# Kernel tuning notes

Measured on AMD Instinct MI355X. Metric: run time of the kernel, lower is better.

Reference implementation:

```python
import jax, jax.numpy as jnp
import numpy as np
from jax import lax

B, T_IN, T_OUT = 32, 256, 500
N_MEL, ENC_DIM = 80, 512
ATT_RNN, DEC_RNN, PRENET, ATT_DIM = 1024, 1024, 256, 128
LOC_F, LOC_K = 32, 31
P_ATT_DROP, P_DEC_DROP = 0.1, 0.1


def setup_inputs() -> dict:
    key = jax.random.key(0)
    ks = jax.random.split(key, 24)
    rn = lambda k, s, sc=0.02: jax.random.normal(k, s, dtype=jnp.float32) * sc
    inp = {}
    inp['memory'] = jax.random.normal(ks[0], (B, T_IN, ENC_DIM), dtype=jnp.float32)
    inp['decoder_inputs'] = jax.random.normal(ks[1], (B, N_MEL, T_OUT), dtype=jnp.float32)
    inp['memory_lengths'] = jax.random.randint(ks[2], (B,), T_IN // 2, T_IN + 1)
    inp['prenet_w1'] = rn(ks[3], (PRENET, N_MEL))
    inp['prenet_w2'] = rn(ks[4], (PRENET, PRENET))
    inp['att_w_ih'] = rn(ks[5], (4 * ATT_RNN, PRENET + ENC_DIM))
    inp['att_w_hh'] = rn(ks[6], (4 * ATT_RNN, ATT_RNN))
    inp['att_b_ih'] = jnp.zeros((4 * ATT_RNN,), jnp.float32)
    inp['att_b_hh'] = jnp.zeros((4 * ATT_RNN,), jnp.float32)
    inp['query_w'] = rn(ks[7], (ATT_DIM, ATT_RNN))
    inp['memory_w'] = rn(ks[8], (ATT_DIM, ENC_DIM))
    inp['v_w'] = rn(ks[9], (1, ATT_DIM))
    inp['loc_conv_w'] = rn(ks[10], (LOC_F, 2, LOC_K))
    inp['loc_dense_w'] = rn(ks[11], (ATT_DIM, LOC_F))
    inp['dec_w_ih'] = rn(ks[12], (4 * DEC_RNN, ATT_RNN + ENC_DIM))
    inp['dec_w_hh'] = rn(ks[13], (4 * DEC_RNN, DEC_RNN))
    inp['dec_b_ih'] = jnp.zeros((4 * DEC_RNN,), jnp.float32)
    inp['dec_b_hh'] = jnp.zeros((4 * DEC_RNN,), jnp.float32)
    inp['proj_w'] = rn(ks[14], (N_MEL, DEC_RNN + ENC_DIM))
    inp['proj_b'] = jnp.zeros((N_MEL,), jnp.float32)
    inp['gate_w'] = rn(ks[15], (1, DEC_RNN + ENC_DIM))
    inp['gate_b'] = jnp.zeros((1,), jnp.float32)
    return inp


def _lstm_cell(x, h, c, w_ih, w_hh, b_ih, b_hh):
    gates = x @ w_ih.T + b_ih + h @ w_hh.T + b_hh
    i, f, g, o = jnp.split(gates, 4, axis=-1)
    c2 = jax.nn.sigmoid(f) * c + jax.nn.sigmoid(i) * jnp.tanh(g)
    h2 = jax.nn.sigmoid(o) * jnp.tanh(c2)
    return h2, c2


def _dropout_masks():
    # deterministic dropout masks (training=True semantics), keep-prob scaled
    kd = jax.random.key(1)
    k1, k2, k3, k4 = jax.random.split(kd, 4)
    m1 = jax.random.bernoulli(k1, 0.5, (T_OUT + 1, B, PRENET)).astype(jnp.float32) / 0.5
    m2 = jax.random.bernoulli(k2, 0.5, (T_OUT + 1, B, PRENET)).astype(jnp.float32) / 0.5
    ma = jax.random.bernoulli(k3, 1 - P_ATT_DROP, (T_OUT, B, ATT_RNN)).astype(jnp.float32) / (1 - P_ATT_DROP)
    md = jax.random.bernoulli(k4, 1 - P_DEC_DROP, (T_OUT, B, DEC_RNN)).astype(jnp.float32) / (1 - P_DEC_DROP)
    return m1, m2, ma, md


def _decode(memory, decoder_inputs, memory_lengths, prenet_w1, prenet_w2,
            att_w_ih, att_w_hh, att_b_ih, att_b_hh, query_w, memory_w, v_w,
            loc_conv_w, loc_dense_w, dec_w_ih, dec_w_hh, dec_b_ih, dec_b_hh,
            proj_w, proj_b, gate_w, gate_b):
    pm1, pm2, att_drop, dec_drop = _dropout_masks()
    processed_memory = jnp.einsum('bte,ae->bta', memory, memory_w)  # (B,T_in,128)
    pad_mask = jnp.arange(T_IN)[None, :] >= memory_lengths[:, None]  # True = padded

    # teacher-forced decoder inputs: (B,n_mel,T) -> (T,B,n_mel), prepend go frame
    dec_in = jnp.transpose(decoder_inputs, (2, 0, 1))
    dec_in = jnp.concatenate([jnp.zeros((1, B, N_MEL), dec_in.dtype), dec_in], 0)
    # prenet (relu + dropout p=0.5, always training)
    x = jax.nn.relu(dec_in @ prenet_w1.T) * pm1
    x = jax.nn.relu(x @ prenet_w2.T) * pm2
    prenet_out = x[:T_OUT]  # (T,B,256)

    pad = (LOC_K - 1) // 2

    def attention(att_h, aw, aw_cum):
        pq = att_h @ query_w.T  # (B,128)
        awc = jnp.stack([aw, aw_cum], axis=1)  # (B,2,T_in)
        loc = lax.conv_general_dilated(awc, loc_conv_w, (1,), [(pad, pad)],
                                       dimension_numbers=('NCH', 'OIH', 'NCH'))  # (B,32,T_in)
        loc = jnp.einsum('bft,af->bta', loc, loc_dense_w)  # (B,T_in,128)
        energies = jnp.tanh(pq[:, None, :] + loc + processed_memory) @ v_w[0]  # (B,T_in)
        energies = jnp.where(pad_mask, -jnp.inf, energies)
        w = jax.nn.softmax(energies, axis=1)
        ctx = jnp.einsum('bt,bte->be', w, memory)  # (B,512)
        return ctx, w

    def step(carry, xs):
        ah, ac, dh, dc, aw, aw_cum, ctx = carry
        pn, adm, ddm = xs
        cell_in = jnp.concatenate([pn, ctx], axis=-1)  # (B,768)
        ah, ac = _lstm_cell(cell_in, ah, ac, att_w_ih, att_w_hh, att_b_ih, att_b_hh)
        ah = ah * adm
        ctx, aw = attention(ah, aw, aw_cum)
        aw_cum = aw_cum + aw
        din = jnp.concatenate([ah, ctx], axis=-1)  # (B,1536)
        dh, dc = _lstm_cell(din, dh, dc, dec_w_ih, dec_w_hh, dec_b_ih, dec_b_hh)
        dh = dh * ddm
        dhac = jnp.concatenate([dh, ctx], axis=-1)  # (B,1536)
        mel = dhac @ proj_w.T + proj_b  # (B,80)
        gate = (dhac @ gate_w.T + gate_b)[:, 0]  # (B,)
        return (ah, ac, dh, dc, aw, aw_cum, ctx), (mel, gate, aw)

    z = lambda d: jnp.zeros((B, d), jnp.float32)
    init = (z(ATT_RNN), z(ATT_RNN), z(DEC_RNN), z(DEC_RNN),
            jnp.zeros((B, T_IN), jnp.float32), jnp.zeros((B, T_IN), jnp.float32), z(ENC_DIM))
    _, (mels, gates, aligns) = lax.scan(step, init, (prenet_out, att_drop, dec_drop))

    mel_outputs = jnp.transpose(mels, (1, 2, 0))   # (B, n_mel, T_out)
    gate_outputs = gates.T                          # (B, T_out)
    alignments = jnp.transpose(aligns, (1, 0, 2))   # (B, T_out, T_in)
    return mel_outputs, gate_outputs, alignments


def reference(memory, decoder_inputs, memory_lengths, prenet_w1, prenet_w2,
              att_w_ih, att_w_hh, att_b_ih, att_b_hh, query_w, memory_w, v_w,
              loc_conv_w, loc_dense_w, dec_w_ih, dec_w_hh, dec_b_ih, dec_b_hh,
              proj_w, proj_b, gate_w, gate_b):
    return _decode(memory, decoder_inputs, memory_lengths, prenet_w1, prenet_w2,
                   att_w_ih, att_w_hh, att_b_ih, att_b_hh, query_w, memory_w, v_w,
                   loc_conv_w, loc_dense_w, dec_w_ih, dec_w_hh, dec_b_ih, dec_b_hh,
                   proj_w, proj_b, gate_w, gate_b)
```

## Files before the change

kernel.cpp:

```cpp
#include <hip/hip_runtime.h>
#include <math.h>
#include <string.h>

#define TOUT 500
#define AOFF 1296000
#define GOFF 1280000
#define TF_BITS_XOR 1

typedef float f32x4 __attribute__((ext_vector_type(4)));
typedef short bf16x8 __attribute__((ext_vector_type(8)));
typedef unsigned short ushort4_t __attribute__((ext_vector_type(4)));
typedef unsigned u32x4 __attribute__((ext_vector_type(4)));

struct Params {
  const float *memory, *dec_in, *pw1, *pw2, *awih, *awhh, *abih, *abhh;
  const float *qw, *mw, *vw, *lcw, *ldw, *dwih, *dwhh, *dbih, *dbhh;
  const float *pjw, *pjb, *gw, *gb;
  const int* mlen;
  float* out;
  unsigned short *ahb0, *ahb1, *dhb0, *dhb1, *ctxb0, *ctxb1;
  unsigned *slots;
  unsigned *flags;
  float *x1, *w1t, *w2t, *mwt, *ldwt, *ba, *bd;
  unsigned short *pre_bf, *pm_bf, *mem_t, *qw_bf, *wpa, *wpd;
  unsigned *mma, *mmd, *mm1, *mm2;
};

__host__ __device__ inline void tf_block(unsigned k0, unsigned k1, unsigned x0, unsigned x1,
                                         unsigned& o0, unsigned& o1) {
  unsigned ks2 = k0 ^ k1 ^ 0x1BD11BDAu;
  x0 += k0; x1 += k1;
#define TFR(r) { x0 += x1; x1 = (x1 << r) | (x1 >> (32 - r)); x1 ^= x0; }
  TFR(13) TFR(15) TFR(26) TFR(6)
  x0 += k1;  x1 += ks2 + 1u;
  TFR(17) TFR(29) TFR(16) TFR(24)
  x0 += ks2; x1 += k0 + 2u;
  TFR(13) TFR(15) TFR(26) TFR(6)
  x0 += k0;  x1 += k1 + 3u;
  TFR(17) TFR(29) TFR(16) TFR(24)
  x0 += k1;  x1 += ks2 + 4u;
  TFR(13) TFR(15) TFR(26) TFR(6)
  x0 += ks2; x1 += k0 + 5u;
#undef TFR
  o0 = x0; o1 = x1;
}

__device__ inline float sigf(float x) { return 1.f / (1.f + __expf(-x)); }
__device__ inline float tanh_fast(float x) {
  float ax = fabsf(x);
  float t = __expf(-2.f * ax);
  float r = (1.f - t) / (1.f + t);
  return copysignf(r, x);
}
__device__ inline unsigned short f2bf(float f) {
  unsigned u = __float_as_uint(f);
  unsigned r = (u + 0x7FFFu + ((u >> 16) & 1u)) >> 16;
  return (unsigned short)r;
}
__device__ inline float bf2f(unsigned short u) {
  return __uint_as_float((unsigned)u << 16);
}

__device__ inline unsigned long long ld_coh64(const void* ptr) {
  return __hip_atomic_load((unsigned long long*)ptr, __ATOMIC_RELAXED, __HIP_MEMORY_SCOPE_SYSTEM);
}
__device__ inline unsigned ld_coh32(const unsigned* ptr) {
  return __hip_atomic_load(ptr, __ATOMIC_RELAXED, __HIP_MEMORY_SCOPE_SYSTEM);
}
__device__ inline void st_coh32(unsigned* ptr, unsigned v) {
  __hip_atomic_store(ptr, v, __ATOMIC_RELAXED, __HIP_MEMORY_SCOPE_SYSTEM);
}

template<bool COH>
__device__ __forceinline__ u32x4 ld16(const void* ptr) {
  u32x4 r;
// ... 143 lines not shown
  int b = wg >> 4, tc = wg & 15;
  int tid = threadIdx.x;
  int t0 = tc * 16;
  for (int idx = tid; idx < 16 * 512; idx += 128) {
    int i = idx >> 9, k = idx & 511;
    mrows[i][k] = p.memory[((size_t)b * 256 + t0 + i) * 512 + k];
  }
  __syncthreads();
  float acc[16];
#pragma unroll
  for (int i = 0; i < 16; ++i) acc[i] = 0.f;
  for (int k = 0; k < 512; ++k) {
    float wv = p.mwt[k * 128 + tid];
#pragma unroll
    for (int i = 0; i < 16; ++i) acc[i] += mrows[i][k] * wv;
  }
  for (int i = 0; i < 16; ++i)
    p.pm_bf[((size_t)b * 256 + t0 + i) * 128 + tid] = f2bf(acc[i]);
}

template<int LEN, bool COH>
struct Seg {
  static constexpr int CPR = LEN / 8;
  static constexpr int N = (32 * CPR) / 512;
  u32x4 r[N];
  __device__ __forceinline__ void load(const unsigned short* src, int srcStride, int tid) {
#pragma unroll
    for (int i = 0; i < N; ++i) {
      int idx = tid + i * 512;
      int b = idx / CPR, c = idx % CPR;
      r[i] = ld16<COH>(src + (size_t)b * srcStride + c * 8);
    }
  }
  __device__ __forceinline__ void store(unsigned short* dst, int dstOff, int dstStride, int tid) {
#pragma unroll
    for (int i = 0; i < N; ++i) {
      int idx = tid + i * 512;
      int b = idx / CPR, c = idx % CPR;
      *(u32x4*)(dst + b * dstStride + dstOff + c * 8) = r[i];
    }
  }
};

__device__ __forceinline__ void drain_vm() {
  asm volatile("s_waitcnt vmcnt(0)" ::: "memory");
  __builtin_amdgcn_sched_barrier(0);
}

#define MFMA_BF16(a, b, c) __builtin_amdgcn_mfma_f32_16x16x32_bf16(a, b, c, 0, 0, 0)

template<int NC, int CPW, int P0J, bool ATT>
__device__ __forceinline__ void gemm_tile2(const Params& p, const bf16x8* bfa, const bf16x8* bfb,
                                           int lane, int v, int s,
                                           const unsigned short* ctxb_prev,
                                           const unsigned short* ahb_prev,
                                           const unsigned short* dhb_prev2,
                                           unsigned short* Abuf, float* pl, int tid) {
  const int arow = lane & 15;
  const int kgrp = (lane >> 4) * 8;
  f32x4 acc00 = {0,0,0,0}, acc01 = {0,0,0,0}, acc10 = {0,0,0,0}, acc11 = {0,0,0,0};

  const int RS0 = ATT ? 776 : 1288;
  if (ATT) {
    Seg<256, false> s0; Seg<512, true> s1;
    s0.load(p.pre_bf + (size_t)s * 32 * 256, 256, tid);
    s1.load(ctxb_prev, 512, tid);
    drain_vm();
    s0.store(Abuf, 0, RS0, tid);
    s1.store(Abuf, 256, RS0, tid);
  } else {
    Seg<1024, true> s0; Seg<256, true> s1;
    s0.load(ahb_prev, 1024, tid);
    s1.load(ctxb_prev, 512, tid);
    drain_vm();
    s0.store(Abuf, 0, RS0, tid);
    s1.store(Abuf, 1024, RS0, tid);
  }
  __syncthreads();
#pragma unroll
  for (int j = 0; j < P0J; ++j) {
    const int kc = (v + 8 * j) * 32;
    const int off = arow * RS0 + kc + kgrp;
    bf16x8 a0 = *(const bf16x8*)&Abuf[off];
    bf16x8 a1 = *(const bf16x8*)&Abuf[off + 16 * RS0];
    acc00 = MFMA_BF16(a0, bfa[j], acc00);
    acc01 = MFMA_BF16(a1, bfa[j], acc01);
    acc10 = MFMA_BF16(a0, bfb[j], acc10);
    acc11 = MFMA_BF16(a1, bfb[j], acc11);
  }
  __syncthreads();

  const int RS1 = ATT ? 1032 : 1288;
  if (ATT) {
    Seg<1024, true> s0;
    s0.load(ahb_prev, 1024, tid);
    drain_vm();
    s0.store(Abuf, 0, RS1, tid);
  } else {
    Seg<256, true> s0; Seg<1024, true> s1;
    s0.load(ctxb_prev + 256, 512, tid);
    s1.load(dhb_prev2, 1024, tid);
    drain_vm();
    s0.store(Abuf, 0, RS1, tid);
    s1.store(Abuf, 256, RS1, tid);
  }
  __syncthreads();
  const int K1 = ATT ? 768 : 1280;
#pragma unroll
  for (int j = P0J; j < CPW; ++j) {
    const int kc = (v + 8 * j) * 32 - K1;
    const int off = arow * RS1 + kc + kgrp;
    bf16x8 a0 = *(const bf16x8*)&Abuf[off];
    bf16x8 a1 = *(const bf16x8*)&Abuf[off + 16 * RS1];
    acc00 = MFMA_BF16(a0, bfa[j], acc00);
    acc01 = MFMA_BF16(a1, bfa[j], acc01);
    acc10 = MFMA_BF16(a0, bfb[j], acc10);
    acc11 = MFMA_BF16(a1, bfb[j], acc11);
  }
  __syncthreads();

  const int po = (lane & 15) * 17 + (lane >> 4) * 4;
#pragma unroll
  for (int j = 0; j < 4; ++j) {
    pl[v * 1088 +   0 + po + j] = acc00[j];
    pl[v * 1088 + 272 + po + j] = acc01[j];
    pl[v * 1088 + 544 + po + j] = acc10[j];
    pl[v * 1088 + 816 + po + j] = acc11[j];
  }
}

template<bool MASTER>
__device__ __forceinline__ void gbar(const Params& p, int wg, int tid, unsigned bargen) {
  __syncthreads();
  if (MASTER) {
    if (tid == 0) st_coh32(p.slots + wg * 32, bargen);
    for (;;) {
      int ok = 1;
      if (tid < 256) ok = (ld_coh32(p.slots + tid * 32) >= bargen) ? 1 : 0;
      if (__syncthreads_count(ok) == 512) break;
      __builtin_amdgcn_s_sleep(1);
    }
    if (tid < 8) st_coh32(p.flags + tid * 32, bargen);
  } else {
    if (tid == 0) {
      st_coh32(p.slots + wg * 32, bargen);
      while (ld_coh32(p.flags + (wg & 7) * 32) < bargen)
        __builtin_amdgcn_s_sleep(2);
    }
    __syncthreads();
  }
}

template<bool IS_ATT, bool MASTER>
__device__ __forceinline__ void run_scan(const Params& p, int wg, int tid,
                                         unsigned short* Abuf, float* pl, float* gates,
                                         float* cst, float* aw_l, float* awc_l, float* sm,
                                         unsigned short* ahst, unsigned short* cxst,
                                         unsigned short* hst) {
  const int lane = tid & 63;
  const int v = tid >> 6;
  constexpr int NC  = IS_ATT ? 56 : 80;
  constexpr int CPW = IS_ATT ? 7 : 10;
  constexpr int P0J = IS_ATT ? 3 : 5;
  const int wgl = IS_ATT ? wg : (wg - 128);
  const int Tb  = wgl * 2;

  bf16x8 bfa[CPW], bfb[CPW];
  {
    const unsigned short* wp = IS_ATT ? p.wpa : p.wpd;
#pragma unroll
    for (int j = 0; j < CPW; ++j) {
      const int c = v + 8 * j;
      const unsigned short* bp = wp + ((size_t)(Tb * NC + c) * 64 + lane) * 8;
      bfa[j] = *(const bf16x8*)bp;
      bfb[j] = *(const bf16x8*)(bp + (size_t)NC * 64 * 8);
    }
  }

  float pjr[48];
  int melb = 0, melc7 = 0, melm0 = 0, melmc = 0;
  {
    if (wg >= 32) {
      int idx = wg - 32;
      melb = idx / 7; melc7 = idx % 7;
      melm0 = melc7 * 12; melmc = (melc7 == 6) ? 8 : 12;
      int mi = tid >> 5, kg = tid & 31;
      if (mi < melmc) {
        const float* pw = p.pjw + (size_t)(melm0 + mi) * 1536 + kg * 48;
#pragma unroll
        for (int j = 0; j < 48; ++j) pjr[j] = pw[j];
      }
    }
  }

  unsigned bargen = 0;

  for (int s = 0; s <= 500; ++s) {
    const int sb = s & 1;
    const unsigned short* ahb_prev  = sb ? p.ahb0 : p.ahb1;
    unsigned short*       ahb_cur   = sb ? p.ahb1 : p.ahb0;
    const unsigned short* dhb_prev2 = sb ? p.dhb1 : p.dhb0;
    unsigned short*       dhb_out   = sb ? p.dhb0 : p.dhb1;
    const unsigned short* ctxb_prev = sb ? p.ctxb0 : p.ctxb1;
    unsigned short*       ctxb_cur  = sb ? p.ctxb1 : p.ctxb0;

    const bool gemm_on = IS_ATT ? (s < 500) : (s >= 1);

    if (gemm_on)
      gemm_tile2<NC, CPW, P0J, IS_ATT>(p, bfa, bfb, lane, v, s, ctxb_prev, ahb_prev, dhb_prev2, Abuf, pl, tid);
    __syncthreads();
    if (gemm_on) {
      const float* bias = IS_ATT ? p.ba : p.bd;
      const int nb32 = wgl * 32;
#pragma unroll
      for (int rep = 0; rep < 2; ++rep) {
        int o = rep * 512 + tid;
        int tile = o >> 9, half = (o >> 8) & 1, n = (o >> 4) & 15, brow = o & 15;
        int o2 = (tile * 2 + half) * 272 + n * 17 + brow;
        float acc = 0.f;
#pragma unroll
        for (int w = 0; w < 8; ++w) acc += pl[w * 1088 + o2];
        int n_local = tile * 16 + n;
        gates[n_local * 33 + half * 16 + brow] = acc + bias[nb32 + n_local];
      }
    }
    __syncthreads();
    if (gemm_on && tid < 256) {
      int u_local = tid >> 5, b = tid & 31;
      float gi = gates[(u_local * 4 + 0) * 33 + b];
      float gf = gates[(u_local * 4 + 1) * 33 + b];
      float gg = gates[(u_local * 4 + 2) * 33 + b];
      float go = gates[(u_local * 4 + 3) * 33 + b];
      float I = sigf(gi), F = sigf(gf), G = tanh_fast(gg), O = sigf(go);
      float c2 = F * cst[tid] + I * G;
      float h = O * tanh_fast(c2);
      cst[tid] = c2;
      int u = wgl * 8 + u_local;
      float mv;
      if (IS_ATT) {
        unsigned e = ((unsigned)s * 32 + b) * 1024u + u;
        mv = ((p.mma[e >> 5] >> (e & 31)) & 1u) ? (1.f / 0.9f) : 0.f;
      } else {
        unsigned e = ((unsigned)(s - 1) * 32 + b) * 1024u + u;
        mv = ((p.mmd[e >> 5] >> (e & 31)) & 1u) ? (1.f / 0.9f) : 0.f;
      }
      hst[tid] = f2bf(h * mv);
    }
    __syncthreads();
    if (gemm_on && tid < 128) {
      int j = tid >> 5, bb = tid & 31;
      unsigned lo = hst[j * 64 + bb], hi = hst[j * 64 + 32 + bb];
      unsigned val = lo | (hi << 16);
      unsigned short* basep = IS_ATT ? ahb_cur : dhb_out;
      int T8 = wgl * 8;
      st_coh32((unsigned*)(basep + (size_t)bb * 1024 + T8 + 2 * j), val);
    }

    gbar<MASTER>(p, wg, tid, ++bargen);

    if (IS_ATT && wg < 32) {
      if (s < 500) {
        const int b = wg;
        unsigned short* locT_bf = (unsigned short*)pl;
        float* ldwt_l = (float*)((char*)(void*)pl + 16640);
        {
          const float4* srcw = (const float4*)p.ldwt;
          float4* dstw = (float4*)ldwt_l;
          dstw[tid] = srcw[tid];
          dstw[tid + 512] = srcw[tid + 512];
        }
        if (tid < 256) {
          unsigned long long q = ld_coh64((const unsigned long long*)(ahb_cur + (size_t)b * 1024) + tid);
          *(unsigned long long*)&ahst[tid * 4] = q;
        }
#pragma unroll
        for (int rep = 0; rep < 4; ++rep) {
          int qd = rep * 512 + tid;
          int f = qd >> 6, tq = (qd & 63) * 4;
          const float* wf = p.lcw + f * 62;
          float w[36]; float acc[4] = {0, 0, 0, 0};
#pragma unroll
          for (int j2 = 0; j2 < 9; ++j2) {
            float4 x = *(const float4*)&aw_l[tq + j2 * 4];
            w[j2*4] = x.x; w[j2*4+1] = x.y; w[j2*4+2] = x.z; w[j2*4+3] = x.w;
          }
#pragma unroll
          for (int k = 0; k < 31; ++k) {
            float cc = wf[k];
            acc[0] += w[k+1]*cc; acc[1] += w[k+2]*cc; acc[2] += w[k+3]*cc; acc[3] += w[k+4]*cc;
          }
#pragma unroll
          for (int j2 = 0; j2 < 9; ++j2) {
            float4 x = *(const float4*)&awc_l[tq + j2 * 4];
            w[j2*4] = x.x; w[j2*4+1] = x.y; w[j2*4+2] = x.z; w[j2*4+3] = x.w;
          }
#pragma unroll
          for (int k = 0; k < 31; ++k) {
            float cc = wf[31 + k];
            acc[0] += w[k+1]*cc; acc[1] += w[k+2]*cc; acc[2] += w[k+3]*cc; acc[3] += w[k+4]*cc;
          }
#pragma unroll
          for (int j2 = 0; j2 < 4; ++j2) locT_bf[f * 260 + tq + j2] = f2bf(acc[j2]);
        }
        __syncthreads();
        {
          int a = tid & 127, kq = tid >> 7;
          const unsigned short* qp = p.qw_bf + (size_t)a * 1024 + kq * 256;
          float acc = 0.f;
#pragma unroll 4
          for (int j = 0; j < 256; j += 8) {
            bf16x8 qv = *(const bf16x8*)(qp + j);
            bf16x8 av = *(const bf16x8*)&ahst[kq * 256 + j];
#pragma unroll
            for (int j2 = 0; j2 < 8; ++j2)
              acc += bf2f((unsigned short)av[j2]) * bf2f((unsigned short)qv[j2]);
          }
          sm[256 + kq * 128 + a] = acc;
          if (tid < 128) sm[128 + tid] = p.vw[tid];
        }
        __syncthreads();
        if (tid < 128) sm[tid] = sm[256 + tid] + sm[384 + tid] + sm[512 + tid] + sm[640 + tid];
        __syncthreads();
        {
          int t = tid & 255, h2 = tid >> 8;
          float lt[32];
#pragma unroll
          for (int f = 0; f < 32; ++f) lt[f] = bf2f(locT_bf[f * 260 + t]);
          const unsigned short* pmp = p.pm_bf + ((size_t)b * 256 + t) * 128;
          float e = 0.f;
#pragma unroll 2
          for (int ac = 0; ac < 16; ++ac) {
            int a0 = h2 * 64 + ac * 4;
            float4 l2 = {0, 0, 0, 0};
#pragma unroll
            for (int f = 0; f < 32; ++f) {
              float4 wv = *(const float4*)&ldwt_l[f * 128 + a0];
              l2.x += lt[f]*wv.x; l2.y += lt[f]*wv.y; l2.z += lt[f]*wv.z; l2.w += lt[f]*wv.w;
            }
            ushort4_t pv = *(const ushort4_t*)(pmp + a0);
            e += tanh_fast(sm[a0+0] + l2.x + bf2f(pv.x)) * sm[128+a0+0];
            e += tanh_fast(sm[a0+1] + l2.y + bf2f(pv.y)) * sm[128+a0+1];
            e += tanh_fast(sm[a0+2] + l2.z + bf2f(pv.z)) * sm[128+a0+2];
            e += tanh_fast(sm[a0+3] + l2.w + bf2f(pv.w)) * sm[128+a0+3];
          }
          sm[256 + h2 * 256 + t] = e;
        }
        __syncthreads();
        if (tid < 256) {
          float en = sm[256 + tid] + sm[512 + tid];
          float w = (tid < p.mlen[b]) ? __expf(en) : 0.f;
          sm[768 + tid] = w;
        }
        __syncthreads();
        if (tid < 32) {
          float sub = 0.f;
#pragma unroll
          for (int i = 0; i < 8; ++i) sub += sm[768 + tid * 8 + i];
          sm[256 + tid] = sub;
        }
        __syncthreads();
        if (tid == 0) {
          float S = 0.f;
#pragma unroll
          for (int i = 0; i < 32; ++i) S += sm[256 + i];
          sm[1281] = 1.f / S;
        }
        __syncthreads();
        if (tid < 256) {
          float awv = sm[768 + tid] * sm[1281];
          aw_l[16 + tid] = awv;
          awc_l[16 + tid] += awv;
          p.out[(size_t)AOFF + (size_t)b * 128000 + (size_t)s * 256 + tid] = awv;
          sm[1024 + tid] = awv;
        }
        __syncthreads();
        {
          const unsigned short* mt = p.mem_t + (size_t)b * 131072 + (size_t)tid * 256;
          float acc = 0.f;
#pragma unroll 8
          for (int t2 = 0; t2 < 256; t2 += 8) {
            bf16x8 mv = *(const bf16x8*)(mt + t2);
#pragma unroll
            for (int j2 = 0; j2 < 8; ++j2)
              acc += sm[1024 + t2 + j2] * bf2f((unsigned short)mv[j2]);
          }
          cxst[tid] = f2bf(acc);
        }
        __syncthreads();
        if (tid < 256) {
          unsigned val = (unsigned)cxst[2 * tid] | ((unsigned)cxst[2 * tid + 1] << 16);
          st_coh32((unsigned*)(ctxb_cur + (size_t)b * 512 + 2 * tid), val);
        }
      }
    } else if (wg >= 32) {
      if (s >= 1) {
        if (tid < 384) {
          unsigned long long q;
          if (tid < 256) q = ld_coh64((const unsigned long long*)(dhb_out + (size_t)melb * 1024) + tid);
          else           q = ld_coh64((const unsigned long long*)(ctxb_prev + (size_t)melb * 512) + (tid - 256));
          *(unsigned long long*)&ahst[tid * 4] = q;
        }
        __syncthreads();
        int mi = tid >> 5, kg = tid & 31;
        if (mi < melmc) {
          float acc = 0.f;
#pragma unroll
          for (int j = 0; j < 48; ++j) acc += bf2f(ahst[kg * 48 + j]) * pjr[j];
          sm[mi * 32 + kg] = acc;
        }
        if (melc7 == 6 && tid >= 384) {
          int kg2 = tid - 384;
          const float* gwp = p.gw + kg2 * 12;
          float acc = 0.f;
#pragma unroll
          for (int j = 0; j < 12; ++j) acc += bf2f(ahst[kg2 * 12 + j]) * gwp[j];
          sm[512 + kg2] = acc;
        }
        __syncthreads();
        if (tid < melmc) {
          float r = p.pjb[melm0 + tid];
#pragma unroll
          for (int j = 0; j < 32; ++j) r += sm[tid * 32 + j];
          p.out[(size_t)melb * 40000 + (size_t)(melm0 + tid) * 500 + (s - 1)] = r;
        }
        if (melc7 == 6 && tid == 384) {
          float r = p.gb[0];
#pragma unroll
          for (int j = 0; j < 128; ++j) r += sm[512 + j];
          p.out[(size_t)GOFF + (size_t)melb * 500 + (s - 1)] = r;
        }
      }
    }

    gbar<MASTER>(p, wg, tid, ++bargen);
  }
}

__global__ void __launch_bounds__(512, 1) scan_kernel(Params p) {
  const int wg = blockIdx.x;
  const int tid = threadIdx.x;

  __shared__ __align__(16) unsigned short Abuf[32 * 1288];
  float* pl = (float*)Abuf;
  __shared__ float gates[32 * 33];
  __shared__ float cst[256];
  __shared__ float aw_l[292], awc_l[292];
  __shared__ float sm[1536];
  __shared__ unsigned short ahst[1536];
  __shared__ unsigned short cxst[512];
  __shared__ unsigned short hst[256];

  if (tid < 256) cst[tid] = 0.f;
  if (tid < 292) { aw_l[tid] = 0.f; awc_l[tid] = 0.f; }

  if (wg < 128) {
    if (wg == 32) run_scan<true, true >(p, wg, tid, Abuf, pl, gates, cst, aw_l, awc_l, sm, ahst, cxst, hst);
    else          run_scan<true, false>(p, wg, tid, Abuf, pl, gates, cst, aw_l, awc_l, sm, ahst, cxst, hst);
  } else {
    run_scan<false, false>(p, wg, tid, Abuf, pl, gates, cst, aw_l, awc_l, sm, ahst, cxst, hst);
  }
}

extern "C" void kernel_launch(void* const* d_in, const int* in_sizes, int n_in,
                              void* d_out, int out_size, void* d_ws, size_t ws_size,
                              hipStream_t stream) {
  Params p;
  p.memory = (const float*)d_in[0];
  p.dec_in = (const float*)d_in[1];
  p.mlen   = (const int*)d_in[2];
  p.pw1  = (const float*)d_in[3];
  p.pw2  = (const float*)d_in[4];
  p.awih = (const float*)d_in[5];
  p.awhh = (const float*)d_in[6];
  p.abih = (const float*)d_in[7];
  p.abhh = (const float*)d_in[8];
  p.qw   = (const float*)d_in[9];
  p.mw   = (const float*)d_in[10];
  p.vw   = (const float*)d_in[11];
  p.lcw  = (const float*)d_in[12];
  p.ldw  = (const float*)d_in[13];
  p.dwih = (const float*)d_in[14];
  p.dwhh = (const float*)d_in[15];
  p.dbih = (const float*)d_in[16];
  p.dbhh = (const float*)d_in[17];
  p.pjw  = (const float*)d_in[18];
  p.pjb  = (const float*)d_in[19];
  p.gw   = (const float*)d_in[20];
  p.gb   = (const float*)d_in[21];
  p.out  = (float*)d_out;

  char* cur = (char*)d_ws;
  auto allocf = [&](size_t n) { float* r = (float*)cur; cur += n * sizeof(float); return r; };
  auto allocs = [&](size_t n) { unsigned short* r = (unsigned short*)cur; cur += n * sizeof(unsigned short); return r; };
  p.ahb0 = allocs(32 * 1024); p.ahb1 = allocs(32 * 1024);
  p.dhb0 = allocs(32 * 1024); p.dhb1 = allocs(32 * 1024);
  p.ctxb0 = allocs(32 * 512); p.ctxb1 = allocs(32 * 512);
  p.slots = (unsigned*)cur; cur += 256 * 32 * sizeof(unsigned);
  p.flags = (unsigned*)cur; cur += 8 * 32 * sizeof(unsigned);
  size_t state_bytes = (size_t)(cur - (char*)d_ws);
  p.x1   = allocf((size_t)500 * 32 * 256);
  p.w1t  = allocf(80 * 256);
  p.w2t  = allocf(256 * 256);
  p.mwt  = allocf(512 * 128);
  p.ldwt = allocf(32 * 128);
  p.ba   = allocf(4096);
  p.bd   = allocf(4096);
  p.pre_bf  = allocs((size_t)500 * 32 * 256);
  p.pm_bf   = allocs((size_t)32 * 256 * 128);
  p.mem_t   = allocs((size_t)32 * 512 * 256);
  p.qw_bf   = allocs(128 * 1024);
  p.wpa     = allocs((size_t)256 * 56 * 64 * 8);
  p.wpd     = allocs((size_t)256 * 80 * 64 * 8);
  p.mma = (unsigned*)cur; cur += 512000u * 4;
  p.mmd = (unsigned*)cur; cur += 512000u * 4;
  p.mm1 = (unsigned*)cur; cur += 128256u * 4;
  p.mm2 = (unsigned*)cur; cur += 128256u * 4;

  (void)hipMemsetAsync(d_ws, 0, state_bytes, stream);

  unsigned k[8];
  {
    unsigned o0, o1;
    tf_block(0u, 1u, 0u, 0u, o0, o1); k[0] = o0; k[1] = o1;
    tf_block(0u, 1u, 0u, 1u, o0, o1); k[2] = o0; k[3] = o1;
    tf_block(0u, 1u, 0u, 2u, o0, o1); k[4] = o0; k[5] = o1;
    tf_block(0u, 1u, 0u, 3u, o0, o1); k[6] = o0; k[7] = o1;
  }

  maskgen_kernel<<<(1280512 + 255) / 256, 256, 0, stream>>>(p, k[0], k[1], k[2], k[3], k[4], k[5], k[6], k[7]);
  prep_misc<<<(4489216 + 255) / 256, 256, 0, stream>>>(p);
  pack_att<<<(917504 + 255) / 256, 256, 0, stream>>>(p);
  pack_dec<<<(1310720 + 255) / 256, 256, 0, stream>>>(p);
  prenet1_kernel<<<2000, 256, 0, stream>>>(p);
  prenet2_kernel<<<2000, 256, 0, stream>>>(p);
  pm_kernel<<<512, 128, 0, stream>>>(p);

  void* args[] = { (void*)&p };
  (void)hipLaunchCooperativeKernel((const void*)scan_kernel, dim3(256), dim3(512), args, 0, stream);
}
```

Measured before the change: 35.82 ms.

## Decouple attention and decoder workgroups with separate barriers and step flags

The single 256-workgroup grid barrier per step is replaced by two independent 128-workgroup barriers, one for the attention LSTM group and one for the decoder LSTM group. Cross-group progress flags (attflag/decflag) let the attention side run up to one step ahead of the decoder, so the decoder GEMM for step i can overlap with attention work for step i+1. The mel/gate projection moves onto the decoder workgroups, split 4 per batch and reading weights from global memory instead of registers. This removes the lockstep stalls but adds flag polling, and correctness now depends on the double-buffer distance holding.

```diff
diff --git a/kernel.cpp b/kernel.cpp
--- a/kernel.cpp
+++ b/kernel.cpp
@@ -20,7 +20,10 @@
   float* out;
   unsigned short *ahb0, *ahb1, *dhb0, *dhb1, *ctxb0, *ctxb1;
   unsigned *slots;
-  unsigned *flags;
+  unsigned *abf;
+  unsigned *dbf;
+  unsigned *attflag;
+  unsigned *decflag;
   float *x1, *w1t, *w2t, *mwt, *ldwt, *ba, *bd;
   unsigned short *pre_bf, *pm_bf, *mem_t, *qw_bf, *wpa, *wpd;
   unsigned *mma, *mmd, *mm1, *mm2;
@@ -270,9 +273,9 @@
 template<int NC, int CPW, int P0J, bool ATT>
 __device__ __forceinline__ void gemm_tile2(const Params& p, const bf16x8* bfa, const bf16x8* bfb,
                                            int lane, int v, int s,
-                                           const unsigned short* ctxb_prev,
-                                           const unsigned short* ahb_prev,
-                                           const unsigned short* dhb_prev2,
+                                           const unsigned short* ctxb_in,
+                                           const unsigned short* ahb_in,
+                                           const unsigned short* dhb_in,
                                            unsigned short* Abuf, float* pl, int tid) {
   const int arow = lane & 15;
   const int kgrp = (lane >> 4) * 8;
@@ -282,14 +285,14 @@
   if (ATT) {
     Seg<256, false> s0; Seg<512, true> s1;
     s0.load(p.pre_bf + (size_t)s * 32 * 256, 256, tid);
-    s1.load(ctxb_prev, 512, tid);
+    s1.load(ctxb_in, 512, tid);
     drain_vm();
     s0.store(Abuf, 0, RS0, tid);
     s1.store(Abuf, 256, RS0, tid);
   } else {
     Seg<1024, true> s0; Seg<256, true> s1;
-    s0.load(ahb_prev, 1024, tid);
-    s1.load(ctxb_prev, 512, tid);
+    s0.load(ahb_in, 1024, tid);
+    s1.load(ctxb_in, 512, tid);
     drain_vm();
     s0.store(Abuf, 0, RS0, tid);
     s1.store(Abuf, 1024, RS0, tid);
@@ -311,13 +314,13 @@
   const int RS1 = ATT ? 1032 : 1288;
   if (ATT) {
     Seg<1024, true> s0;
-    s0.load(ahb_prev, 1024, tid);
+    s0.load(ahb_in, 1024, tid);
     drain_vm();
     s0.store(Abuf, 0, RS1, tid);
   } else {
     Seg<256, true> s0; Seg<1024, true> s1;
-    s0.load(ctxb_prev + 256, 512, tid);
-    s1.load(dhb_prev2, 1024, tid);
+    s0.load(ctxb_in + 256, 512, tid);
+    s1.load(dhb_in, 1024, tid);
     drain_vm();
     s0.store(Abuf, 0, RS1, tid);
     s1.store(Abuf, 256, RS1, tid);
@@ -347,310 +350,337 @@
   }
 }
 
+template<bool ATT>
+__device__ __forceinline__ void lstm_tail(const Params& p, int wgl, int tid, unsigned step,
+                                          unsigned short* hout, float* pl, float* gates,
+                                          float* cst, unsigned short* hst) {
+  __syncthreads();
+  {
+    const float* bias = ATT ? p.ba : p.bd;
+    const int nb32 = wgl * 32;
+#pragma unroll
+    for (int rep = 0; rep < 2; ++rep) {
+      int o = rep * 512 + tid;
+      int tile = o >> 9, half = (o >> 8) & 1, n = (o >> 4) & 15, brow = o & 15;
+      int o2 = (tile * 2 + half) * 272 + n * 17 + brow;
+      float acc = 0.f;
+#pragma unroll
+      for (int w = 0; w < 8; ++w) acc += pl[w * 1088 + o2];
+      int n_local = tile * 16 + n;
+      gates[n_local * 33 + half * 16 + brow] = acc + bias[nb32 + n_local];
+    }
+  }
+  __syncthreads();
+  if (tid < 256) {
+    int u_local = tid >> 5, b = tid & 31;
+    float gi = gates[(u_local * 4 + 0) * 33 + b];
+    float gf = gates[(u_local * 4 + 1) * 33 + b];
+    float gg = gates[(u_local * 4 + 2) * 33 + b];
+    float go = gates[(u_local * 4 + 3) * 33 + b];
+    float I = sigf(gi), F = sigf(gf), G = tanh_fast(gg), O = sigf(go);
+    float c2 = F * cst[tid] + I * G;
+    float h = O * tanh_fast(c2);
+    cst[tid] = c2;
+    int u = wgl * 8 + u_local;
+    const unsigned* maskw = ATT ? p.mma : p.mmd;
+    unsigned e = (step * 32 + (unsigned)b) * 1024u + (unsigned)u;
+    float mv = ((maskw[e >> 5] >> (e & 31)) & 1u) ? (1.f / 0.9f) : 0.f;
+    hst[tid] = f2bf(h * mv);
+  }
+  __syncthreads();
+  if (tid < 128) {
+    int j = tid >> 5, bb = tid & 31;
+    unsigned lo = hst[j * 64 + bb], hi = hst[j * 64 + 32 + bb];
+    unsigned val = lo | (hi << 16);
+    int T8 = wgl * 8;
+    st_coh32((unsigned*)(hout + (size_t)bb * 1024 + T8 + 2 * j), val);
+  }
+}
+
 template<bool MASTER>
-__device__ __forceinline__ void gbar(const Params& p, int wg, int tid, unsigned bargen) {
+__device__ __forceinline__ void dbar(const Params& p, unsigned* flg, int base, int wg, int tid, unsigned gen) {
   __syncthreads();
   if (MASTER) {
-    if (tid == 0) st_coh32(p.slots + wg * 32, bargen);
+    if (tid == 0) st_coh32(p.slots + (base + (wg & 127)) * 32, gen);
     for (;;) {
       int ok = 1;
-      if (tid < 256) ok = (ld_coh32(p.slots + tid * 32) >= bargen) ? 1 : 0;
+      if (tid < 128) ok = (ld_coh32(p.slots + (base + tid) * 32) >= gen) ? 1 : 0;
       if (__syncthreads_count(ok) == 512) break;
       __builtin_amdgcn_s_sleep(1);
     }
-    if (tid < 8) st_coh32(p.flags + tid * 32, bargen);
+    if (tid < 8) st_coh32(flg + tid * 32, gen);
   } else {
     if (tid == 0) {
-      st_coh32(p.slots + wg * 32, bargen);
-      while (ld_coh32(p.flags + (wg & 7) * 32) < bargen)
+      st_coh32(p.slots + (base + (wg & 127)) * 32, gen);
+      while (ld_coh32(flg + (wg & 7) * 32) < gen)
         __builtin_amdgcn_s_sleep(2);
     }
     __syncthreads();
   }
 }
 
-template<bool IS_ATT, bool MASTER>
-__device__ __forceinline__ void run_scan(const Params& p, int wg, int tid,
-                                         unsigned short* Abuf, float* pl, float* gates,
-                                         float* cst, float* aw_l, float* awc_l, float* sm,
-                                         unsigned short* ahst, unsigned short* cxst,
-                                         unsigned short* hst) {
+template<bool MASTER>
+__device__ void run_att(const Params& p, int wg, int tid,
+                        unsigned short* Abuf, float* pl, float* gates,
+                        float* cst, float* aw_l, float* awc_l, float* sm,
+                        unsigned short* ahst, unsigned short* cxst, unsigned short* hst) {
   const int lane = tid & 63;
   const int v = tid >> 6;
-  constexpr int NC  = IS_ATT ? 56 : 80;
-  constexpr int CPW = IS_ATT ? 7 : 10;
-  constexpr int P0J = IS_ATT ? 3 : 5;
-  const int wgl = IS_ATT ? wg : (wg - 128);
-  const int Tb  = wgl * 2;
-
-  bf16x8 bfa[CPW], bfb[CPW];
-  {
-    const unsigned short* wp = IS_ATT ? p.wpa : p.wpd;
-#pragma unroll
-    for (int j = 0; j < CPW; ++j) {
-      const int c = v + 8 * j;
-      const unsigned short* bp = wp + ((size_t)(Tb * NC + c) * 64 + lane) * 8;
-      bfa[j] = *(const bf16x8*)bp;
-      bfb[j] = *(const bf16x8*)(bp + (size_t)NC * 64 * 8);
-    }
-  }
-
-  float pjr[48];
-  int melb = 0, melc7 = 0, melm0 = 0, melmc = 0;
-  {
-    if (wg >= 32) {
-      int idx = wg - 32;
-      melb = idx / 7; melc7 = idx % 7;
-      melm0 = melc7 * 12; melmc = (melc7 == 6) ? 8 : 12;
-      int mi = tid >> 5, kg = tid & 31;
-      if (mi < melmc) {
-        const float* pw = p.pjw + (size_t)(melm0 + mi) * 1536 + kg * 48;
-#pragma unroll
-        for (int j = 0; j < 48; ++j) pjr[j] = pw[j];
-      }
-    }
-  }
-
-  unsigned bargen = 0;
-
-  for (int s = 0; s <= 500; ++s) {
+  const int Tb = wg * 2;
+
+  bf16x8 bfa[7], bfb[7];
+#pragma unroll
+  for (int j = 0; j < 7; ++j) {
+    const int c = v + 8 * j;
+    const unsigned short* bp = p.wpa + ((size_t)(Tb * 56 + c) * 64 + lane) * 8;
+    bfa[j] = *(const bf16x8*)bp;
+    bfb[j] = *(const bf16x8*)(bp + (size_t)56 * 64 * 8);
+  }
+
+  unsigned gen = 0;
+  for (int s = 0; s < 500; ++s) {
     const int sb = s & 1;
-    const unsigned short* ahb_prev  = sb ? p.ahb0 : p.ahb1;
-    unsigned short*       ahb_cur   = sb ? p.ahb1 : p.ahb0;
-    const unsigned short* dhb_prev2 = sb ? p.dhb1 : p.dhb0;
-    unsigned short*       dhb_out   = sb ? p.dhb0 : p.dhb1;
+    const unsigned short* ahb_prev = sb ? p.ahb0 : p.ahb1;
+    unsigned short*       ahb_cur  = sb ? p.ahb1 : p.ahb0;
     const unsigned short* ctxb_prev = sb ? p.ctxb0 : p.ctxb1;
     unsigned short*       ctxb_cur  = sb ? p.ctxb1 : p.ctxb0;
 
-    const bool gemm_on = IS_ATT ? (s < 500) : (s >= 1);
-
-    if (gemm_on)
-      gemm_tile2<NC, CPW, P0J, IS_ATT>(p, bfa, bfb, lane, v, s, ctxb_prev, ahb_prev, dhb_prev2, Abuf, pl, tid);
+    if (tid == 0) {
+      while ((int)ld_coh32(p.decflag + (wg & 7) * 32) < s - 1)
+        __builtin_amdgcn_s_sleep(4);
+    }
     __syncthreads();
-    if (gemm_on) {
-      const float* bias = IS_ATT ? p.ba : p.bd;
-      const int nb32 = wgl * 32;
+
+    gemm_tile2<56, 7, 3, true>(p, bfa, bfb, lane, v, s, ctxb_prev, ahb_prev, nullptr, Abuf, pl, tid);
+    lstm_tail<true>(p, wg, tid, (unsigned)s, ahb_cur, pl, gates, cst, hst);
+
+    dbar<MASTER>(p, p.abf, 0, wg, tid, ++gen);
+
+    if (wg < 32) {
+      const int b = wg;
+      unsigned short* locT_bf = (unsigned short*)pl;
+      float* ldwt_l = (float*)((char*)(void*)pl + 16640);
+      {
+        const float4* srcw = (const float4*)p.ldwt;
+        float4* dstw = (float4*)ldwt_l;
+        dstw[tid] = srcw[tid];
+        dstw[tid + 512] = srcw[tid + 512];
+      }
+      if (tid < 256) {
+        unsigned long long q = ld_coh64((const unsigned long long*)(ahb_cur + (size_t)b * 1024) + tid);
+        *(unsigned long long*)&ahst[tid * 4] = q;
+      }
+#pragma unroll
+      for (int rep = 0; rep < 4; ++rep) {
+        int qd = rep * 512 + tid;
+        int f = qd >> 6, tq = (qd & 63) * 4;
+        const float* wf = p.lcw + f * 62;
+        float w[36]; float acc[4] = {0, 0, 0, 0};
+#pragma unroll
+        for (int j2 = 0; j2 < 9; ++j2) {
+          float4 x = *(const float4*)&aw_l[tq + j2 * 4];
+          w[j2*4] = x.x; w[j2*4+1] = x.y; w[j2*4+2] = x.z; w[j2*4+3] = x.w;
+        }
+#pragma unroll
+        for (int k = 0; k < 31; ++k) {
+          float cc = wf[k];
+          acc[0] += w[k+1]*cc; acc[1] += w[k+2]*cc; acc[2] += w[k+3]*cc; acc[3] += w[k+4]*cc;
+        }
+#pragma unroll
+        for (int j2 = 0; j2 < 9; ++j2) {
+          float4 x = *(const float4*)&awc_l[tq + j2 * 4];
+          w[j2*4] = x.x; w[j2*4+1] = x.y; w[j2*4+2] = x.z; w[j2*4+3] = x.w;
+        }
+#pragma unroll
+        for (int k = 0; k < 31; ++k) {
+          float cc = wf[31 + k];
+          acc[0] += w[k+1]*cc; acc[1] += w[k+2]*cc; acc[2] += w[k+3]*cc; acc[3] += w[k+4]*cc;
+        }
+#pragma unroll
+        for (int j2 = 0; j2 < 4; ++j2) locT_bf[f * 260 + tq + j2] = f2bf(acc[j2]);
+      }
+      __syncthreads();
+      {
+        int a = tid & 127, kq = tid >> 7;
+        const unsigned short* qp = p.qw_bf + (size_t)a * 1024 + kq * 256;
+        float acc = 0.f;
+#pragma unroll 4
+        for (int j = 0; j < 256; j += 8) {
+          bf16x8 qv = *(const bf16x8*)(qp + j);
+          bf16x8 av = *(const bf16x8*)&ahst[kq * 256 + j];
+#pragma unroll
+          for (int j2 = 0; j2 < 8; ++j2)
+            acc += bf2f((unsigned short)av[j2]) * bf2f((unsigned short)qv[j2]);
+        }
+        sm[256 + kq * 128 + a] = acc;
+        if (tid < 128) sm[128 + tid] = p.vw[tid];
+      }
+      __syncthreads();
+      if (tid < 128) sm[tid] = sm[256 + tid] + sm[384 + tid] + sm[512 + tid] + sm[640 + tid];
+      __syncthreads();
+      {
+        int t = tid & 255, h2 = tid >> 8;
+        float lt[32];
+#pragma unroll
+        for (int f = 0; f < 32; ++f) lt[f] = bf2f(locT_bf[f * 260 + t]);
+        const unsigned short* pmp = p.pm_bf + ((size_t)b * 256 + t) * 128;
+        float e = 0.f;
+#pragma unroll 2
+        for (int ac = 0; ac < 16; ++ac) {
+          int a0 = h2 * 64 + ac * 4;
+          float4 l2 = {0, 0, 0, 0};
+#pragma unroll
+          for (int f = 0; f < 32; ++f) {
+            float4 wv = *(const float4*)&ldwt_l[f * 128 + a0];
+            l2.x += lt[f]*wv.x; l2.y += lt[f]*wv.y; l2.z += lt[f]*wv.z; l2.w += lt[f]*wv.w;
+          }
+          ushort4_t pv = *(const ushort4_t*)(pmp + a0);
+          e += tanh_fast(sm[a0+0] + l2.x + bf2f(pv.x)) * sm[128+a0+0];
+          e += tanh_fast(sm[a0+1] + l2.y + bf2f(pv.y)) * sm[128+a0+1];
+          e += tanh_fast(sm[a0+2] + l2.z + bf2f(pv.z)) * sm[128+a0+2];
+          e += tanh_fast(sm[a0+3] + l2.w + bf2f(pv.w)) * sm[128+a0+3];
+        }
+        sm[256 + h2 * 256 + t] = e;
+      }
+      __syncthreads();
+      if (tid < 256) {
+        float en = sm[256 + tid] + sm[512 + tid];
+        float w = (tid < p.mlen[b]) ? __expf(en) : 0.f;
+        sm[768 + tid] = w;
+      }
+      __syncthreads();
+      if (tid < 32) {
+        float sub = 0.f;
+#pragma unroll
+        for (int i2 = 0; i2 < 8; ++i2) sub += sm[768 + tid * 8 + i2];
+        sm[256 + tid] = sub;
+      }
+      __syncthreads();
+      if (tid == 0) {
+        float S = 0.f;
+#pragma unroll
+        for (int i2 = 0; i2 < 32; ++i2) S += sm[256 + i2];
+        sm[1281] = 1.f / S;
+      }
+      __syncthreads();
+      if (tid < 256) {
+        float awv = sm[768 + tid] * sm[1281];
+        aw_l[16 + tid] = awv;
+        awc_l[16 + tid] += awv;
+        p.out[(size_t)AOFF + (size_t)b * 128000 + (size_t)s * 256 + tid] = awv;
+        sm[1024 + tid] = awv;
+      }
+      __syncthreads();
+      {
+        const unsigned short* mt = p.mem_t + (size_t)b * 131072 + (size_t)tid * 256;
+        float acc = 0.f;
+#pragma unroll 8
+        for (int t2 = 0; t2 < 256; t2 += 8) {
+          bf16x8 mv = *(const bf16x8*)(mt + t2);
+#pragma unroll
+          for (int j2 = 0; j2 < 8; ++j2)
+            acc += sm[1024 + t2 + j2] * bf2f((unsigned short)mv[j2]);
+        }
+        cxst[tid] = f2bf(acc);
+      }
+      __syncthreads();
+      if (tid < 256) {
+        unsigned val = (unsigned)cxst[2 * tid] | ((unsigned)cxst[2 * tid + 1] << 16);
+        st_coh32((unsigned*)(ctxb_cur + (size_t)b * 512 + 2 * tid), val);
+      }
+    }
+
+    dbar<MASTER>(p, p.abf, 0, wg, tid, ++gen);
+
+    if (MASTER && tid < 8) st_coh32(p.attflag + tid * 32, (unsigned)(s + 1));
+  }
+}
+
+template<bool MASTER>
+__device__ void run_dec(const Params& p, int wg, int tid,
+                        unsigned short* Abuf, float* pl, float* gates,
+                        float* cst, float* sm, unsigned short* ahst, unsigned short* hst) {
+  const int lane = tid & 63;
+  const int v = tid >> 6;
+  const int wgl = wg - 128;
+  const int Tb = wgl * 2;
+
+  bf16x8 bfa[10], bfb[10];
+#pragma unroll
+  for (int j = 0; j < 10; ++j) {
+    const int c = v + 8 * j;
+    const unsigned short* bp = p.wpd + ((size_t)(Tb * 80 + c) * 64 + lane) * 8;
+    bfa[j] = *(const bf16x8*)bp;
+    bfb[j] = *(const bf16x8*)(bp + (size_t)80 * 64 * 8);
+  }
+  const int melb = wgl >> 2, melc4 = wgl & 3;
+
+  unsigned gen = 0;
+  for (int i = 0; i < 500; ++i) {
+    const int ib = i & 1;
+    const unsigned short* ahb_i  = ib ? p.ahb1 : p.ahb0;
+    const unsigned short* ctxb_i = ib ? p.ctxb1 : p.ctxb0;
+    const unsigned short* dhb_prev = ib ? p.dhb0 : p.dhb1;
+    unsigned short*       dhb_cur  = ib ? p.dhb1 : p.dhb0;
+
+    if (tid == 0) {
+      while ((int)ld_coh32(p.attflag + (wg & 7) * 32) < i + 1)
+        __builtin_amdgcn_s_sleep(4);
+    }
+    __syncthreads();
+
+    gemm_tile2<80, 10, 5, false>(p, bfa, bfb, lane, v, i, ctxb_i, ahb_i, dhb_prev, Abuf, pl, tid);
+    lstm_tail<false>(p, wgl, tid, (unsigned)i, dhb_cur, pl, gates, cst, hst);
+
+    dbar<MASTER>(p, p.dbf, 128, wg, tid, ++gen);
+
+    {
+      if (tid < 384) {
+        unsigned long long q;
+        if (tid < 256) q = ld_coh64((const unsigned long long*)(dhb_cur + (size_t)melb * 1024) + tid);
+        else           q = ld_coh64((const unsigned long long*)(ctxb_i + (size_t)melb * 512) + (tid - 256));
+        *(unsigned long long*)&ahst[tid * 4] = q;
+      }
+      __syncthreads();
+      int mi = tid >> 5, kg = tid & 31;
 #pragma unroll
       for (int rep = 0; rep < 2; ++rep) {
-        int o = rep * 512 + tid;
-        int tile = o >> 9, half = (o >> 8) & 1, n = (o >> 4) & 15, brow = o & 15;
-        int o2 = (tile * 2 + half) * 272 + n * 17 + brow;
-        float acc = 0.f;
-#pragma unroll
-        for (int w = 0; w < 8; ++w) acc += pl[w * 1088 + o2];
-        int n_local = tile * 16 + n;
-        gates[n_local * 33 + half * 16 + brow] = acc + bias[nb32 + n_local];
-      }
-    }
-    __syncthreads();
-    if (gemm_on && tid < 256) {
-      int u_local = tid >> 5, b = tid & 31;
-      float gi = gates[(u_local * 4 + 0) * 33 + b];
-      float gf = gates[(u_local * 4 + 1) * 33 + b];
-      float gg = gates[(u_local * 4 + 2) * 33 + b];
-      float go = gates[(u_local * 4 + 3) * 33 + b];
-      float I = sigf(gi), F = sigf(gf), G = tanh_fast(gg), O = sigf(go);
-      float c2 = F * cst[tid] + I * G;
-      float h = O * tanh_fast(c2);
-      cst[tid] = c2;
-      int u = wgl * 8 + u_local;
-      float mv;
-      if (IS_ATT) {
-        unsigned e = ((unsigned)s * 32 + b) * 1024u + u;
-        mv = ((p.mma[e >> 5] >> (e & 31)) & 1u) ? (1.f / 0.9f) : 0.f;
-      } else {
-        unsigned e = ((unsigned)(s - 1) * 32 + b) * 1024u + u;
-        mv = ((p.mmd[e >> 5] >> (e & 31)) & 1u) ? (1.f / 0.9f) : 0.f;
-      }
-      hst[tid] = f2bf(h * mv);
-    }
-    __syncthreads();
-    if (gemm_on && tid < 128) {
-      int j = tid >> 5, bb = tid & 31;
-      unsigned lo = hst[j * 64 + bb], hi = hst[j * 64 + 32 + bb];
-      unsigned val = lo | (hi << 16);
-      unsigned short* basep = IS_ATT ? ahb_cur : dhb_out;
-      int T8 = wgl * 8;
-      st_coh32((unsigned*)(basep + (size_t)bb * 1024 + T8 + 2 * j), val);
-    }
-
-    gbar<MASTER>(p, wg, tid, ++bargen);
-
-    if (IS_ATT && wg < 32) {
-      if (s < 500) {
-        const int b = wg;
-        unsigned short* locT_bf = (unsigned short*)pl;
-        float* ldwt_l = (float*)((char*)(void*)pl + 16640);
-        {
-          const float4* srcw = (const float4*)p.ldwt;
-          float4* dstw = (float4*)ldwt_l;
-          dstw[tid] = srcw[tid];
-          dstw[tid + 512] = srcw[tid + 512];
-        }
-        if (tid < 256) {
-          unsigned long long q = ld_coh64((const unsigned long long*)(ahb_cur + (size_t)b * 1024) + tid);
-          *(unsigned long long*)&ahst[tid * 4] = q;
-        }
-#pragma unroll
-        for (int rep = 0; rep < 4; ++rep) {
-          int qd = rep * 512 + tid;
-          int f = qd >> 6, tq = (qd & 63) * 4;
-          const float* wf = p.lcw + f * 62;
-          float w[36]; float acc[4] = {0, 0, 0, 0};
-#pragma unroll
-          for (int j2 = 0; j2 < 9; ++j2) {
-            float4 x = *(const float4*)&aw_l[tq + j2 * 4];
-            w[j2*4] = x.x; w[j2*4+1] = x.y; w[j2*4+2] = x.z; w[j2*4+3] = x.w;
-          }
-#pragma unroll
-          for (int k = 0; k < 31; ++k) {
-            float cc = wf[k];
-            acc[0] += w[k+1]*cc; acc[1] += w[k+2]*cc; acc[2] += w[k+3]*cc; acc[3] += w[k+4]*cc;
-          }
-#pragma unroll
-          for (int j2 = 0; j2 < 9; ++j2) {
-            float4 x = *(const float4*)&awc_l[tq + j2 * 4];
-            w[j2*4] = x.x; w[j2*4+1] = x.y; w[j2*4+2] = x.z; w[j2*4+3] = x.w;
-          }
-#pragma unroll
-          for (int k = 0; k < 31; ++k) {
-            float cc = wf[31 + k];
-            acc[0] += w[k+1]*cc; acc[1] += w[k+2]*cc; acc[2] += w[k+3]*cc; acc[3] += w[k+4]*cc;
-          }
-#pragma unroll
-          for (int j2 = 0; j2 < 4; ++j2) locT_bf[f * 260 + tq + j2] = f2bf(acc[j2]);
-        }
-        __syncthreads();
-        {
-          int a = tid & 127, kq = tid >> 7;
-          const unsigned short* qp = p.qw_bf + (size_t)a * 1024 + kq * 256;
+        int mm = rep * 16 + mi;
+        if (mm < 20) {
+          int m = melc4 * 20 + mm;
+          const float* pw = p.pjw + (size_t)m * 1536 + kg * 48;
           float acc = 0.f;
 #pragma unroll 4
-          for (int j = 0; j < 256; j += 8) {
-            bf16x8 qv = *(const bf16x8*)(qp + j);
-            bf16x8 av = *(const bf16x8*)&ahst[kq * 256 + j];
-#pragma unroll
-            for (int j2 = 0; j2 < 8; ++j2)
-              acc += bf2f((unsigned short)av[j2]) * bf2f((unsigned short)qv[j2]);
-          }
-          sm[256 + kq * 128 + a] = acc;
-          if (tid < 128) sm[128 + tid] = p.vw[tid];
+          for (int j = 0; j < 48; ++j) acc += bf2f(ahst[kg * 48 + j]) * pw[j];
+          sm[mm * 32 + kg] = acc;
         }
-        __syncthreads();
-        if (tid < 128) sm[tid] = sm[256 + tid] + sm[384 + tid] + sm[512 + tid] + sm[640 + tid];
-        __syncthreads();
-        {
-          int t = tid & 255, h2 = tid >> 8;
-          float lt[32];
-#pragma unroll
-          for (int f = 0; f < 32; ++f) lt[f] = bf2f(locT_bf[f * 260 + t]);
-          const unsigned short* pmp = p.pm_bf + ((size_t)b * 256 + t) * 128;
-          float e = 0.f;
-#pragma unroll 2
-          for (int ac = 0; ac < 16; ++ac) {
-            int a0 = h2 * 64 + ac * 4;
-            float4 l2 = {0, 0, 0, 0};
-#pragma unroll
-            for (int f = 0; f < 32; ++f) {
-              float4 wv = *(const float4*)&ldwt_l[f * 128 + a0];
-              l2.x += lt[f]*wv.x; l2.y += lt[f]*wv.y; l2.z += lt[f]*wv.z; l2.w += lt[f]*wv.w;
-            }
-            ushort4_t pv = *(const ushort4_t*)(pmp + a0);
-            e += tanh_fast(sm[a0+0] + l2.x + bf2f(pv.x)) * sm[128+a0+0];
-            e += tanh_fast(sm[a0+1] + l2.y + bf2f(pv.y)) * sm[128+a0+1];
-            e += tanh_fast(sm[a0+2] + l2.z + bf2f(pv.z)) * sm[128+a0+2];
-            e += tanh_fast(sm[a0+3] + l2.w + bf2f(pv.w)) * sm[128+a0+3];
-          }
-          sm[256 + h2 * 256 + t] = e;
-        }
-        __syncthreads();
-        if (tid < 256) {
-          float en = sm[256 + tid] + sm[512 + tid];
-          float w = (tid < p.mlen[b]) ? __expf(en) : 0.f;
-          sm[768 + tid] = w;
-        }
-        __syncthreads();
-        if (tid < 32) {
-          float sub = 0.f;
-#pragma unroll
-          for (int i = 0; i < 8; ++i) sub += sm[768 + tid * 8 + i];
-          sm[256 + tid] = sub;
-        }
-        __syncthreads();
-        if (tid == 0) {
-          float S = 0.f;
-#pragma unroll
-          for (int i = 0; i < 32; ++i) S += sm[256 + i];
-          sm[1281] = 1.f / S;
-        }
-        __syncthreads();
-        if (tid < 256) {
-          float awv = sm[768 + tid] * sm[1281];
-          aw_l[16 + tid] = awv;
-          awc_l[16 + tid] += awv;
-          p.out[(size_t)AOFF + (size_t)b * 128000 + (size_t)s * 256 + tid] = awv;
-          sm[1024 + tid] = awv;
-        }
-        __syncthreads();
-        {
-          const unsigned short* mt = p.mem_t + (size_t)b * 131072 + (size_t)tid * 256;
-          float acc = 0.f;
-#pragma unroll 8
-          for (int t2 = 0; t2 < 256; t2 += 8) {
-            bf16x8 mv = *(const bf16x8*)(mt + t2);
-#pragma unroll
-            for (int j2 = 0; j2 < 8; ++j2)
-              acc += sm[1024 + t2 + j2] * bf2f((unsigned short)mv[j2]);
-          }
-          cxst[tid] = f2bf(acc);
-        }
-        __syncthreads();
-        if (tid < 256) {
-          unsigned val = (unsigned)cxst[2 * tid] | ((unsigned)cxst[2 * tid + 1] << 16);
-          st_coh32((unsigned*)(ctxb_cur + (size_t)b * 512 + 2 * tid), val);
-        }
-      }
-    } else if (wg >= 32) {
-      if (s >= 1) {
-        if (tid < 384) {
-          unsigned long long q;
-          if (tid < 256) q = ld_coh64((const unsigned long long*)(dhb_out + (size_t)melb * 1024) + tid);
-          else           q = ld_coh64((const unsigned long long*)(ctxb_prev + (size_t)melb * 512) + (tid - 256));
-          *(unsigned long long*)&ahst[tid * 4] = q;
-        }
-        __syncthreads();
-        int mi = tid >> 5, kg = tid & 31;
-        if (mi < melmc) {
-          float acc = 0.f;
-#pragma unroll
-          for (int j = 0; j < 48; ++j) acc += bf2f(ahst[kg * 48 + j]) * pjr[j];
-          sm[mi * 32 + kg] = acc;
-        }
-        if (melc7 == 6 && tid >= 384) {
-          int kg2 = tid - 384;
-          const float* gwp = p.gw + kg2 * 12;
-          float acc = 0.f;
-#pragma unroll
-          for (int j = 0; j < 12; ++j) acc += bf2f(ahst[kg2 * 12 + j]) * gwp[j];
-          sm[512 + kg2] = acc;
-        }
-        __syncthreads();
-        if (tid < melmc) {
-          float r = p.pjb[melm0 + tid];
-#pragma unroll
-          for (int j = 0; j < 32; ++j) r += sm[tid * 32 + j];
-          p.out[(size_t)melb * 40000 + (size_t)(melm0 + tid) * 500 + (s - 1)] = r;
-        }
-        if (melc7 == 6 && tid == 384) {
-          float r = p.gb[0];
-#pragma unroll
-          for (int j = 0; j < 128; ++j) r += sm[512 + j];
-          p.out[(size_t)GOFF + (size_t)melb * 500 + (s - 1)] = r;
-        }
-      }
-    }
-
-    gbar<MASTER>(p, wg, tid, ++bargen);
+      }
+      if (melc4 == 3 && tid >= 384) {
+        int kg2 = tid - 384;
+        const float* gwp = p.gw + kg2 * 12;
+        float acc = 0.f;
+#pragma unroll
+        for (int j = 0; j < 12; ++j) acc += bf2f(ahst[kg2 * 12 + j]) * gwp[j];
+        sm[896 + kg2] = acc;
+      }
+      __syncthreads();
+      if (tid < 20) {
+        float r = p.pjb[melc4 * 20 + tid];
+#pragma unroll
+        for (int j = 0; j < 32; ++j) r += sm[tid * 32 + j];
+        p.out[(size_t)melb * 40000 + (size_t)(melc4 * 20 + tid) * 500 + i] = r;
+      }
+      if (melc4 == 3 && tid == 384) {
+        float r = p.gb[0];
+#pragma unroll
+        for (int j = 0; j < 128; ++j) r += sm[896 + j];
+        p.out[(size_t)GOFF + (size_t)melb * 500 + i] = r;
+      }
+    }
+
+    dbar<MASTER>(p, p.dbf, 128, wg, tid, ++gen);
+
+    if (MASTER && tid < 8) st_coh32(p.decflag + tid * 32, (unsigned)(i + 1));
   }
 }
 
@@ -672,10 +702,11 @@
   if (tid < 292) { aw_l[tid] = 0.f; awc_l[tid] = 0.f; }
 
   if (wg < 128) {
-    if (wg == 32) run_scan<true, true >(p, wg, tid, Abuf, pl, gates, cst, aw_l, awc_l, sm, ahst, cxst, hst);
-    else          run_scan<true, false>(p, wg, tid, Abuf, pl, gates, cst, aw_l, awc_l, sm, ahst, cxst, hst);
+    if (wg == 32) run_att<true >(p, wg, tid, Abuf, pl, gates, cst, aw_l, awc_l, sm, ahst, cxst, hst);
+    else          run_att<false>(p, wg, tid, Abuf, pl, gates, cst, aw_l, awc_l, sm, ahst, cxst, hst);
   } else {
-    run_scan<false, false>(p, wg, tid, Abuf, pl, gates, cst, aw_l, awc_l, sm, ahst, cxst, hst);
+    if (wg == 160) run_dec<true >(p, wg, tid, Abuf, pl, gates, cst, sm, ahst, hst);
+    else           run_dec<false>(p, wg, tid, Abuf, pl, gates, cst, sm, ahst, hst);
   }
 }
 
@@ -713,8 +744,11 @@
   p.ahb0 = allocs(32 * 1024); p.ahb1 = allocs(32 * 1024);
   p.dhb0 = allocs(32 * 1024); p.dhb1 = allocs(32 * 1024);
   p.ctxb0 = allocs(32 * 512); p.ctxb1 = allocs(32 * 512);
-  p.slots = (unsigned*)cur; cur += 256 * 32 * sizeof(unsigned);
-  p.flags = (unsigned*)cur; cur += 8 * 32 * sizeof(unsigned);
+  p.slots   = (unsigned*)cur; cur += 256 * 32 * sizeof(unsigned);
+  p.abf     = (unsigned*)cur; cur += 8 * 32 * sizeof(unsigned);
+  p.dbf     = (unsigned*)cur; cur += 8 * 32 * sizeof(unsigned);
+  p.attflag = (unsigned*)cur; cur += 8 * 32 * sizeof(unsigned);
+  p.decflag = (unsigned*)cur; cur += 8 * 32 * sizeof(unsigned);
   size_t state_bytes = (size_t)(cur - (char*)d_ws);
   p.x1   = allocf((size_t)500 * 32 * 256);
   p.w1t  = allocf(80 * 256);
```

New measurement: 34.77 ms. 2.9% less time.
